# Kernel optimization log

Hardware: AMD Instinct MI355X
Metric: run time of the kernel (lower is better)

## Reference

```python
import jax, jax.numpy as jnp
import numpy as np

N_NODES = 100000
N_EDGES = 3200000
IN_F, HID, N_CLS = 512, 16, 7


def setup_inputs() -> dict:
    key = jax.random.key(0)
    k1, k2, k3, k4 = jax.random.split(key, 4)
    x = jax.random.normal(k1, (N_NODES, IN_F), dtype=jnp.float32)
    edge_index = jax.random.randint(k2, (2, N_EDGES), 0, N_NODES, dtype=jnp.int32)
    W1 = jax.random.normal(k3, (IN_F, HID), dtype=jnp.float32) * (1.0 / np.sqrt(IN_F))
    b1 = jnp.zeros((HID,), dtype=jnp.float32)
    W2 = jax.random.normal(k4, (HID, N_CLS), dtype=jnp.float32) * (1.0 / np.sqrt(HID))
    b2 = jnp.zeros((N_CLS,), dtype=jnp.float32)
    return {"x": x, "edge_index": edge_index, "W1": W1, "b1": b1, "W2": W2, "b2": b2}


def _gcn_norm(src, dst, n_nodes):
    # symmetric normalization with self-loops already included in (src, dst)
    deg = jax.ops.segment_sum(jnp.ones(dst.shape, jnp.float32), dst, num_segments=n_nodes)
    dinv = jnp.where(deg > 0, jax.lax.rsqrt(deg), 0.0)
    return dinv[src] * dinv[dst]  # [E]


def _gcn_conv(h, src, dst, norm, W, b, n_nodes):
    # transform-first (PyG GCNConv), then normalized scatter-add aggregation
    h = h @ W                                   # [N, out]
    msg = h[src] * norm[:, None]                # gather + scale, [E, out]
    out = jax.ops.segment_sum(msg, dst, num_segments=n_nodes)  # scatter-add
    return out + b


def reference(x, edge_index, W1, b1, W2, b2):
    n = x.shape[0]
    loops = jnp.arange(n, dtype=edge_index.dtype)
    src = jnp.concatenate([edge_index[0], loops])
    dst = jnp.concatenate([edge_index[1], loops])
    norm = _gcn_norm(src, dst, n)
    h = _gcn_conv(x, src, dst, norm, W1, b1, n)
    h = jax.nn.relu(h)
    out = _gcn_conv(h, src, dst, norm, W2, b2, n)
    return out
```

## Files before the change

kernel.cpp:

```cpp
#include <hip/hip_runtime.h>

#define CHUNK 8192
#define BMAX 512

typedef __attribute__((address_space(3))) unsigned int lds_u32;
typedef const __attribute__((address_space(1))) unsigned int glb_u32;

__device__ __forceinline__ void gload16(const float* g, float* l) {
    __builtin_amdgcn_global_load_lds((glb_u32*)g, (lds_u32*)l, 16, 0, 0);
}


__global__ __launch_bounds__(256) void k_coarse_hist(const int* __restrict__ dst, int E,
                                                     int* __restrict__ bc,
                                                     int* __restrict__ blockBase, int B) {
    __shared__ int cnt[BMAX];
    int t = threadIdx.x;
    cnt[t] = 0; cnt[t + 256] = 0;
    __syncthreads();
    int e0 = blockIdx.x * CHUNK;
#pragma unroll
    for (int it = 0; it < CHUNK / 256; ++it) {
        int e = e0 + it * 256 + t;
        if (e < E) atomicAdd(&cnt[dst[e] >> 8], 1);
    }
    __syncthreads();
    for (int b = t; b < B; b += 256) {
        int c = cnt[b];
        if (c > 0) blockBase[(size_t)blockIdx.x * B + b] = atomicAdd(&bc[b], c);
    }
}

__global__ void k_scan_bsums(int* bsums, int nb) {
    __shared__ int s[2][512];
    int t = threadIdx.x;
    int v = (t < nb) ? bsums[t] : 0;
    int p = 0;
    s[0][t] = v;
    __syncthreads();
    for (int off = 1; off < 512; off <<= 1) {
        s[p ^ 1][t] = s[p][t] + ((t >= off) ? s[p][t - off] : 0);
        p ^= 1;
        __syncthreads();
    }
    if (t < nb) bsums[t] = s[p][t] - v;
}


__global__ __launch_bounds__(256) void k_coarse_scatter(const int* __restrict__ src,
                                                        const int* __restrict__ dst, int E,
                                                        const int* __restrict__ bucketBase,
                                                        const int* __restrict__ blockBase, int B,
                                                        unsigned int* __restrict__ ebuf) {
    __shared__ int run[BMAX];
    int t = threadIdx.x;
    run[t] = 0; run[t + 256] = 0;
    __syncthreads();
    int e0 = blockIdx.x * CHUNK;
#pragma unroll
    for (int it = 0; it < CHUNK / 256; ++it) {
        int e = e0 + it * 256 + t;
        if (e < E) {
            int d = dst[e];
            int b = d >> 8;
            int rank = atomicAdd(&run[b], 1);
            int pos = bucketBase[b] + blockBase[(size_t)blockIdx.x * B + b] + rank;
            ebuf[pos] = ((unsigned int)(d & 255) << 24) | (unsigned int)src[e];
        }
    }
}


__global__ __launch_bounds__(256) void k_bucket_hist(const unsigned int* __restrict__ ebuf,
                                                     const int* __restrict__ bucketBase,
                                                     int E, int N, int B,
                                                     int* __restrict__ hist,
                                                     float* __restrict__ dinv) {
    __shared__ int cnt[256];
    int t = threadIdx.x;
    int b = blockIdx.x;
    cnt[t] = 0;
    __syncthreads();
    int e0 = bucketBase[b];
    int e1 = (b + 1 < B) ? bucketBase[b + 1] : E;
    for (int e = e0 + t; e < e1; e += 256) atomicAdd(&cnt[ebuf[e] >> 24], 1);
    __syncthreads();
    int node = b * 256 + t;
    if (node < N) {
        hist[node] = cnt[t];
        dinv[node] = rsqrtf((float)(cnt[t] + 1));
    }
}


__global__ __launch_bounds__(256) void k_fine_scatter(const unsigned int* __restrict__ ebuf,
                                                      const int* __restrict__ bucketBase,
                                                      const int* __restrict__ hist,
                                                      int E, int N, int B,
                                                      int* __restrict__ rowStart,
                                                      int* __restrict__ csr_src) {
    __shared__ int s[2][256];
    __shared__ int cnt[256];
    int t = threadIdx.x;
    int b = blockIdx.x;
    int node = b * 256 + t;
    int v = (node < N) ? hist[node] : 0;
    int p = 0;
    s[0][t] = v;
    __syncthreads();
    for (int off = 1; off < 256; off <<= 1) {
        s[p ^ 1][t] = s[p][t] + ((t >= off) ? s[p][t - off] : 0);
        p ^= 1;
        __syncthreads();
    }
    int rs = bucketBase[b] + s[p][t] - v;
    if (node < N) rowStart[node] = rs;
    cnt[t] = rs;
    __syncthreads();
    int e0 = bucketBase[b];
    int e1 = (b + 1 < B) ? bucketBase[b + 1] : E;
    for (int e = e0 + t; e < e1; e += 256) {
        unsigned int w = ebuf[e];
        int pos = atomicAdd(&cnt[w >> 24], 1);
        csr_src[pos] = (int)(w & 0xFFFFFFu);
    }
}


__global__ __launch_bounds__(256, 6) void k_gemm1(const float* __restrict__ x,
                                                  const float* __restrict__ W1,
                                                  const float* __restrict__ dinv,
                                                  int N, float* __restrict__ h1) {
    __shared__ float xs[2][2048];
    const int t = threadIdx.x;
    const int lane = t & 63;
    const int cq = __builtin_amdgcn_readfirstlane(t >> 6);
    const int R0 = blockIdx.x * 64;

    const float* gbase[2];
#pragma unroll
    for (int u = 0; u < 2; ++u) {
        int r = (cq * 2 + u) * 8 + (lane >> 3);
        int g = lane & 7;
        int row = R0 + r;
        if (row >= N) row = N - 1;
        gbase[u] = x + (size_t)row * 512 + ((g ^ (r & 7)) << 2);
    }

    float acc[4] = {0.f, 0.f, 0.f, 0.f};

#pragma unroll
    for (int u = 0; u < 2; ++u)
        gload16(gbase[u], &xs[0][((cq * 2 + u) * 64 + lane) * 4]);
    __syncthreads();

    const int row = lane;
    const int rs = row & 7;
    int p = 0;
    for (int ch = 0; ch < 16; ++ch) {
        if (ch + 1 < 16) {
#pragma unroll
            for (int u = 0; u < 2; ++u)
                gload16(gbase[u] + (ch + 1) * 32, &xs[p ^ 1][((cq * 2 + u) * 64 + lane) * 4]);
        }
        const float* xr = &xs[p][row * 32];
#pragma unroll
        for (int j = 0; j < 8; ++j) {
            int j4 = (j + cq * 2) & 7;
            float4 xv = *(const float4*)(xr + ((j4 ^ rs) << 2));
            float xe[4] = {xv.x, xv.y, xv.z, xv.w};
            int k = ch * 32 + j4 * 4;
#pragma unroll
            for (int d = 0; d < 4; ++d) {
                const float* wp = W1 + (k + d) * 16 + cq * 4;
#pragma unroll
                for (int c = 0; c < 4; ++c) acc[c] = fmaf(xe[d], wp[c], acc[c]);
            }
        }
        __syncthreads();
        p ^= 1;
    }

    int orow = R0 + row;
    if (orow < N) {
        float di = dinv[orow];
        *(float4*)(h1 + (size_t)orow * 16 + cq * 4) =
            make_float4(acc[0] * di, acc[1] * di, acc[2] * di, acc[3] * di);
    }
}


__global__ void k_gather1(const float* __restrict__ h1, const int* __restrict__ csr_src,
                          const int* __restrict__ rowStart, const int* __restrict__ hist,
                          const float* __restrict__ dinv, const float* __restrict__ b1,
                          int N, float* __restrict__ relu1) {
    int g = blockIdx.x * blockDim.x + threadIdx.x;
    int i = g >> 4, c = g & 15;
    if (i >= N) return;
    float ssum = h1[(size_t)i * 16 + c];
    int e0 = rowStart[i], e1 = e0 + hist[i];
    for (int e = e0; e < e1; ++e) {
        int s = csr_src[e];
        ssum += h1[(size_t)s * 16 + c];
    }
    float v = fmaf(dinv[i], ssum, b1[c]);
    relu1[(size_t)i * 16 + c] = fmaxf(v, 0.0f);
}


__global__ void k_h2(const float* __restrict__ relu1, const float* __restrict__ W2,
                     const float* __restrict__ dinv, int N, float* __restrict__ h2) {
    int i = blockIdx.x * blockDim.x + threadIdx.x;
    if (i >= N) return;
    float r[16];
#pragma unroll
    for (int q = 0; q < 4; ++q) {
        float4 v = *(const float4*)(relu1 + (size_t)i * 16 + q * 4);
        r[q * 4 + 0] = v.x; r[q * 4 + 1] = v.y; r[q * 4 + 2] = v.z; r[q * 4 + 3] = v.w;
    }
    float di = dinv[i];
#pragma unroll
    for (int c2 = 0; c2 < 7; ++c2) {
        float a = 0.0f;
#pragma unroll
        for (int c = 0; c < 16; ++c) a = fmaf(r[c], W2[c * 7 + c2], a);
        h2[(size_t)i * 7 + c2] = a * di;
    }
}


__global__ void k_gather2(const float* __restrict__ h2, const int* __restrict__ csr_src,
                          const int* __restrict__ rowStart, const int* __restrict__ hist,
                          const float* __restrict__ dinv, const float* __restrict__ b2,
                          int N, float* __restrict__ out) {
    int g = blockIdx.x * blockDim.x + threadIdx.x;
    int i = g >> 3, c = g & 7;
    if (i >= N || c >= 7) return;
    float ssum = h2[(size_t)i * 7 + c];
    int e0 = rowStart[i], e1 = e0 + hist[i];
    for (int e = e0; e < e1; ++e) {
        int s = csr_src[e];
        ssum += h2[(size_t)s * 7 + c];
    }
    out[(size_t)i * 7 + c] = fmaf(dinv[i], ssum, b2[c]);
}


extern "C" void kernel_launch(void* const* d_in, const int* in_sizes, int n_in,
                              void* d_out, int out_size, void* d_ws, size_t ws_size,
                              hipStream_t stream) {
    const float* x  = (const float*)d_in[0];
    const int*   ei = (const int*)d_in[1];
    const float* W1 = (const float*)d_in[2];
    const float* b1 = (const float*)d_in[3];
    const float* W2 = (const float*)d_in[4];
    const float* b2 = (const float*)d_in[5];
    float* out = (float*)d_out;

    const int N = in_sizes[0] / 512;
    const int E = in_sizes[1] / 2;
    const int* src = ei;
    const int* dst = ei + E;

    const int nb  = (N + 255) / 256;
    const int B   = nb;
    const int nbA = (E + CHUNK - 1) / CHUNK;
    const int nb64 = (N + 63) / 64;

    char* ws = (char*)d_ws;
    auto alloc = [&](size_t bytes) {
        char* p = ws;
        ws += (bytes + 511) & ~(size_t)511;
        return p;
    };
    int*   hist      = (int*)alloc((size_t)N * 4);
    float* dinv      = (float*)alloc((size_t)N * 4);
    int*   rowStart  = (int*)alloc((size_t)N * 4);
    int*   bc        = (int*)alloc((size_t)(B + 1) * 4);
    int*   blockBase = (int*)alloc((size_t)nbA * B * 4);
    int*   csr_src   = (int*)alloc((size_t)E * 4);
    size_t featBytes = (size_t)N * 16 * 4 * 2 + (size_t)N * 7 * 4;
    size_t ebufBytes = (size_t)E * 4;
    char* regB = alloc(featBytes > ebufBytes ? featBytes : ebufBytes);
    unsigned int* ebuf = (unsigned int*)regB;
    float* h1    = (float*)regB;
    float* relu1 = h1 + (size_t)N * 16;
    float* h2    = relu1 + (size_t)N * 16;

    hipMemsetAsync(bc, 0, (size_t)B * 4, stream);
    k_coarse_hist<<<nbA, 256, 0, stream>>>(dst, E, bc, blockBase, B);
    k_scan_bsums<<<1, 512, 0, stream>>>(bc, B);
    k_coarse_scatter<<<nbA, 256, 0, stream>>>(src, dst, E, bc, blockBase, B, ebuf);
    k_bucket_hist<<<B, 256, 0, stream>>>(ebuf, bc, E, N, B, hist, dinv);
    k_fine_scatter<<<B, 256, 0, stream>>>(ebuf, bc, hist, E, N, B, rowStart, csr_src);
    k_gemm1<<<nb64, 256, 0, stream>>>(x, W1, dinv, N, h1);
    k_gather1<<<(N * 16 + 255) / 256, 256, 0, stream>>>(h1, csr_src, rowStart, hist, dinv, b1, N, relu1);
    k_h2<<<nb, 256, 0, stream>>>(relu1, W2, dinv, N, h2);
    k_gather2<<<(N * 8 + 255) / 256, 256, 0, stream>>>(h2, csr_src, rowStart, hist, dinv, b2, N, out);
}
```

Baseline: 558.7 us.

## Fuse layer-1 gather with W2 transform, pad h2 to 8, unroll gathers

The layer-1 aggregation kernel now applies ReLU and multiplies by W2 in place, using a 16-lane shuffle reduction, and writes a padded 8-wide h2. This removes the separate k_h2 kernel and the relu1 round trip through memory. The second gather reads the padded 8-float rows so each node's row is aligned, which costs some extra bytes per row. Both gather loops are unrolled by four to keep more independent loads in flight.

```diff
diff --git a/kernel.cpp b/kernel.cpp
--- a/kernel.cpp
+++ b/kernel.cpp
@@ -190,59 +190,65 @@
 }
 
 
-__global__ void k_gather1(const float* __restrict__ h1, const int* __restrict__ csr_src,
-                          const int* __restrict__ rowStart, const int* __restrict__ hist,
-                          const float* __restrict__ dinv, const float* __restrict__ b1,
-                          int N, float* __restrict__ relu1) {
+__global__ void k_gather1h2(const float* __restrict__ h1, const int* __restrict__ csr_src,
+                            const int* __restrict__ rowStart, const int* __restrict__ hist,
+                            const float* __restrict__ dinv, const float* __restrict__ b1,
+                            const float* __restrict__ W2, int N,
+                            float* __restrict__ h2p) {
     int g = blockIdx.x * blockDim.x + threadIdx.x;
     int i = g >> 4, c = g & 15;
     if (i >= N) return;
     float ssum = h1[(size_t)i * 16 + c];
-    int e0 = rowStart[i], e1 = e0 + hist[i];
-    for (int e = e0; e < e1; ++e) {
-        int s = csr_src[e];
-        ssum += h1[(size_t)s * 16 + c];
-    }
-    float v = fmaf(dinv[i], ssum, b1[c]);
-    relu1[(size_t)i * 16 + c] = fmaxf(v, 0.0f);
-}
-
-
-__global__ void k_h2(const float* __restrict__ relu1, const float* __restrict__ W2,
-                     const float* __restrict__ dinv, int N, float* __restrict__ h2) {
-    int i = blockIdx.x * blockDim.x + threadIdx.x;
-    if (i >= N) return;
-    float r[16];
-#pragma unroll
-    for (int q = 0; q < 4; ++q) {
-        float4 v = *(const float4*)(relu1 + (size_t)i * 16 + q * 4);
-        r[q * 4 + 0] = v.x; r[q * 4 + 1] = v.y; r[q * 4 + 2] = v.z; r[q * 4 + 3] = v.w;
-    }
+    int e = rowStart[i], e1 = e + hist[i];
+    for (; e + 4 <= e1; e += 4) {
+        int s0 = csr_src[e], s1 = csr_src[e + 1], s2 = csr_src[e + 2], s3 = csr_src[e + 3];
+        float a0 = h1[(size_t)s0 * 16 + c];
+        float a1 = h1[(size_t)s1 * 16 + c];
+        float a2 = h1[(size_t)s2 * 16 + c];
+        float a3 = h1[(size_t)s3 * 16 + c];
+        ssum += (a0 + a1) + (a2 + a3);
+    }
+    for (; e < e1; ++e) ssum += h1[(size_t)csr_src[e] * 16 + c];
+
     float di = dinv[i];
-#pragma unroll
-    for (int c2 = 0; c2 < 7; ++c2) {
-        float a = 0.0f;
-#pragma unroll
-        for (int c = 0; c < 16; ++c) a = fmaf(r[c], W2[c * 7 + c2], a);
-        h2[(size_t)i * 7 + c2] = a * di;
-    }
-}
-
-
-__global__ void k_gather2(const float* __restrict__ h2, const int* __restrict__ csr_src,
+    float v = fmaxf(fmaf(di, ssum, b1[c]), 0.0f);
+
+    float p0 = v * W2[c * 7 + 0], p1 = v * W2[c * 7 + 1], p2 = v * W2[c * 7 + 2],
+          p3 = v * W2[c * 7 + 3], p4 = v * W2[c * 7 + 4], p5 = v * W2[c * 7 + 5],
+          p6 = v * W2[c * 7 + 6];
+#pragma unroll
+    for (int m = 1; m < 16; m <<= 1) {
+        p0 += __shfl_xor(p0, m); p1 += __shfl_xor(p1, m); p2 += __shfl_xor(p2, m);
+        p3 += __shfl_xor(p3, m); p4 += __shfl_xor(p4, m); p5 += __shfl_xor(p5, m);
+        p6 += __shfl_xor(p6, m);
+    }
+    if (c < 8) {
+        float o = (c == 0) ? p0 : (c == 1) ? p1 : (c == 2) ? p2 : (c == 3) ? p3
+                : (c == 4) ? p4 : (c == 5) ? p5 : (c == 6) ? p6 : 0.0f;
+        h2p[(size_t)i * 8 + c] = o * di;
+    }
+}
+
+
+__global__ void k_gather2(const float* __restrict__ h2p, const int* __restrict__ csr_src,
                           const int* __restrict__ rowStart, const int* __restrict__ hist,
                           const float* __restrict__ dinv, const float* __restrict__ b2,
                           int N, float* __restrict__ out) {
     int g = blockIdx.x * blockDim.x + threadIdx.x;
     int i = g >> 3, c = g & 7;
-    if (i >= N || c >= 7) return;
-    float ssum = h2[(size_t)i * 7 + c];
-    int e0 = rowStart[i], e1 = e0 + hist[i];
-    for (int e = e0; e < e1; ++e) {
-        int s = csr_src[e];
-        ssum += h2[(size_t)s * 7 + c];
-    }
-    out[(size_t)i * 7 + c] = fmaf(dinv[i], ssum, b2[c]);
+    if (i >= N) return;
+    float ssum = h2p[(size_t)i * 8 + c];
+    int e = rowStart[i], e1 = e + hist[i];
+    for (; e + 4 <= e1; e += 4) {
+        int s0 = csr_src[e], s1 = csr_src[e + 1], s2 = csr_src[e + 2], s3 = csr_src[e + 3];
+        float a0 = h2p[(size_t)s0 * 8 + c];
+        float a1 = h2p[(size_t)s1 * 8 + c];
+        float a2 = h2p[(size_t)s2 * 8 + c];
+        float a3 = h2p[(size_t)s3 * 8 + c];
+        ssum += (a0 + a1) + (a2 + a3);
+    }
+    for (; e < e1; ++e) ssum += h2p[(size_t)csr_src[e] * 8 + c];
+    if (c < 7) out[(size_t)i * 7 + c] = fmaf(dinv[i], ssum, b2[c]);
 }
 
 
@@ -262,9 +268,9 @@
     const int* src = ei;
     const int* dst = ei + E;
 
-    const int nb  = (N + 255) / 256;
-    const int B   = nb;
-    const int nbA = (E + CHUNK - 1) / CHUNK;
+    const int nb   = (N + 255) / 256;
+    const int B    = nb;
+    const int nbA  = (E + CHUNK - 1) / CHUNK;
     const int nb64 = (N + 63) / 64;
 
     char* ws = (char*)d_ws;
@@ -279,13 +285,12 @@
     int*   bc        = (int*)alloc((size_t)(B + 1) * 4);
     int*   blockBase = (int*)alloc((size_t)nbA * B * 4);
     int*   csr_src   = (int*)alloc((size_t)E * 4);
-    size_t featBytes = (size_t)N * 16 * 4 * 2 + (size_t)N * 7 * 4;
+    size_t featBytes = (size_t)N * 16 * 4 + (size_t)N * 8 * 4;
     size_t ebufBytes = (size_t)E * 4;
     char* regB = alloc(featBytes > ebufBytes ? featBytes : ebufBytes);
     unsigned int* ebuf = (unsigned int*)regB;
-    float* h1    = (float*)regB;
-    float* relu1 = h1 + (size_t)N * 16;
-    float* h2    = relu1 + (size_t)N * 16;
+    float* h1  = (float*)regB;
+    float* h2p = h1 + (size_t)N * 16;
 
     hipMemsetAsync(bc, 0, (size_t)B * 4, stream);
     k_coarse_hist<<<nbA, 256, 0, stream>>>(dst, E, bc, blockBase, B);
@@ -294,7 +299,8 @@
     k_bucket_hist<<<B, 256, 0, stream>>>(ebuf, bc, E, N, B, hist, dinv);
     k_fine_scatter<<<B, 256, 0, stream>>>(ebuf, bc, hist, E, N, B, rowStart, csr_src);
     k_gemm1<<<nb64, 256, 0, stream>>>(x, W1, dinv, N, h1);
-    k_gather1<<<(N * 16 + 255) / 256, 256, 0, stream>>>(h1, csr_src, rowStart, hist, dinv, b1, N, relu1);
-    k_h2<<<nb, 256, 0, stream>>>(relu1, W2, dinv, N, h2);
-    k_gather2<<<(N * 8 + 255) / 256, 256, 0, stream>>>(h2, csr_src, rowStart, hist, dinv, b2, N, out);
-}
+    k_gather1h2<<<(N * 16 + 255) / 256, 256, 0, stream>>>(h1, csr_src, rowStart, hist,
+                                                          dinv, b1, W2, N, h2p);
+    k_gather2<<<(N * 8 + 255) / 256, 256, 0, stream>>>(h2p, csr_src, rowStart, hist,
+                                                       dinv, b2, N, out);
+}
```

Result: faster. 499.0 us (-10.7%).
